# Performance work log

Hardware: AMD Instinct MI355X
Metric: run time of the kernel (lower is better)

The kernel has to match this reference:

```python
import jax, jax.numpy as jnp
import numpy as np

IN_F = 4096
OUT_F = 4096
RANK = 32
GROUP = 64  # int4 weight quantization group size along in_features


def setup_inputs() -> dict:
    key = jax.random.key(0)
    k_x, k_w, k_s, k_ld, k_lu, k_b = jax.random.split(key, 6)
    x = jax.random.normal(k_x, (4096, IN_F), dtype=jnp.float32)
    # int4 weight codes in [-8, 7], stored as int32
    qweight = jax.random.randint(k_w, (OUT_F, IN_F), -8, 8, dtype=jnp.int32)
    # per-(out_channel, group) scales
    wscale = jax.random.uniform(k_s, (OUT_F, IN_F // GROUP), dtype=jnp.float32, minval=0.01, maxval=0.05)
    # low-rank SVD correction branch (LoRA-style)
    lora_down = jax.random.normal(k_ld, (RANK, IN_F), dtype=jnp.float32) * 0.02
    lora_up = jax.random.normal(k_lu, (OUT_F, RANK), dtype=jnp.float32) * 0.02
    bias = jax.random.normal(k_b, (OUT_F,), dtype=jnp.float32) * 0.01
    return {"x": x, "qweight": qweight, "wscale": wscale,
            "lora_down": lora_down, "lora_up": lora_up, "bias": bias}


def reference(x, qweight, wscale, lora_down, lora_up, bias):
    out_f, in_f = qweight.shape
    # dequantize int4 weights group-wise: W[o, g*G+i] = q * scale[o, g]
    W = (qweight.astype(jnp.float32).reshape(out_f, in_f // GROUP, GROUP)
         * wscale[:, :, None]).reshape(out_f, in_f)
    # per-token symmetric int4 activation quantization (W4A4 main path)
    ascale = jnp.maximum(jnp.max(jnp.abs(x), axis=-1, keepdims=True), 1e-6) / 7.0
    xq = jnp.clip(jnp.round(x / ascale), -8.0, 7.0) * ascale  # fake-quantized x
    # main quantized GEMM
    main = jnp.einsum('ti,oi->to', xq, W)
    # low-rank correction uses full-precision activations
    lora = jnp.einsum('tr,or->to', jnp.einsum('ti,ri->tr', x, lora_down), lora_up)
    return main + lora + bias[None, :]
```

## Files before the change

kernel.cpp:

```cpp
#include <hip/hip_runtime.h>

typedef __bf16 bf16x8 __attribute__((ext_vector_type(8)));
typedef float f32x4 __attribute__((ext_vector_type(4)));
typedef unsigned short u16;

#define IN_F 4096
#define OUT_F 4096
#define NTOK 4096
#define RANK 32
#define KEXT 4160
#define NT 65
#define ROWB ((size_t)KEXT * 2)
#define D1 65536

__device__ __forceinline__ u16 f2bf(float f) {
  union { float f; unsigned u; } c; c.f = f;
  unsigned u = c.u;
  return (u16)((u + 0x7FFFu + ((u >> 16) & 1u)) >> 16);
}

__device__ __forceinline__ void gload_lds16(const void* g, void* l) {
  __builtin_amdgcn_global_load_lds((const __attribute__((address_space(1))) void*)g,
                                   (__attribute__((address_space(3))) void*)l,
                                   16, 0, 0);
}

__global__ __launch_bounds__(256) void prep_kernel(const float* __restrict__ x,
                                                   u16* __restrict__ A,
                                                   float* __restrict__ ascale) {
  int t = blockIdx.x;
  int tid = threadIdx.x;
  const float4* xr = (const float4*)(x + (size_t)t * IN_F);
  float4 v[4];
  float m = 0.f;
#pragma unroll
  for (int i = 0; i < 4; ++i) {
    v[i] = xr[tid + i * 256];
    m = fmaxf(m, fmaxf(fmaxf(fabsf(v[i].x), fabsf(v[i].y)),
                       fmaxf(fabsf(v[i].z), fabsf(v[i].w))));
  }
#pragma unroll
  for (int off = 32; off > 0; off >>= 1) m = fmaxf(m, __shfl_xor(m, off));
  __shared__ float wmax[4];
  if ((tid & 63) == 0) wmax[tid >> 6] = m;
  __syncthreads();
  m = fmaxf(fmaxf(wmax[0], wmax[1]), fmaxf(wmax[2], wmax[3]));
  float as = fmaxf(m, 1e-6f) / 7.f;
  float inv = 1.f / as;
  if (tid == 0) ascale[t] = as;
  u16* Ar = A + (size_t)t * KEXT;
#pragma unroll
  for (int i = 0; i < 4; ++i) {
    float q0 = fminf(fmaxf(rintf(v[i].x * inv), -8.f), 7.f);
    float q1 = fminf(fmaxf(rintf(v[i].y * inv), -8.f), 7.f);
    float q2 = fminf(fmaxf(rintf(v[i].z * inv), -8.f), 7.f);
    float q3 = fminf(fmaxf(rintf(v[i].w * inv), -8.f), 7.f);
    ushort4 u;
    u.x = f2bf(q0); u.y = f2bf(q1); u.z = f2bf(q2); u.w = f2bf(q3);
    *(ushort4*)(Ar + (size_t)(tid + i * 256) * 4) = u;
  }
  if (tid < 8) {
    ushort4 z; z.x = z.y = z.z = z.w = 0;
    *(ushort4*)(Ar + IN_F + 32 + tid * 4) = z;
  }
}

__global__ __launch_bounds__(256) void dequant_kernel(const int* __restrict__ qw,
                                                      const float* __restrict__ wscale,
                                                      const float* __restrict__ lu,
                                                      u16* __restrict__ B) {
  int o = blockIdx.x;
  int tid = threadIdx.x;
  const int4* qr = (const int4*)(qw + (size_t)o * IN_F);
  const float* sr = wscale + (size_t)o * (IN_F / 64);
  u16* Br = B + (size_t)o * KEXT;
#pragma unroll
  for (int s = 0; s < 4; ++s) {
    int e = tid + s * 256;
    int4 q = qr[e];
    float sc = sr[e >> 4];
    ushort4 u;
    u.x = f2bf((float)q.x * sc);
    u.y = f2bf((float)q.y * sc);
    u.z = f2bf((float)q.z * sc);
    u.w = f2bf((float)q.w * sc);
    *(ushort4*)(Br + (size_t)4 * e) = u;
  }
  if (tid < RANK) Br[IN_F + tid] = f2bf(lu[(size_t)o * RANK + tid]);
  if (tid < 8) {
    ushort4 z; z.x = z.y = z.z = z.w = 0;
    *(ushort4*)(Br + IN_F + 32 + tid * 4) = z;
  }
}

__global__ __launch_bounds__(256) void lorad_kernel(const float* __restrict__ x,
                                                    const float* __restrict__ ld,
                                                    float* __restrict__ tr8) {
  __shared__ float Xs[128][68];
  __shared__ float Ls[32][68];
  int b = blockIdx.x;
  int t0 = (b >> 3) * 128;
  int kbase = (b & 7) * 512;
  int tid = threadIdx.x;
  int rb = tid & 7;
  int tb = tid >> 3;
  float acc[4][4];
#pragma unroll
  for (int i = 0; i < 4; ++i)
#pragma unroll
    for (int j = 0; j < 4; ++j) acc[i][j] = 0.f;

  for (int kc = 0; kc < 512; kc += 64) {
    int k0 = kbase + kc;
    __syncthreads();
#pragma unroll
    for (int s = 0; s < 8; ++s) {
      int e = tid + s * 256;
      int row = e >> 4, c4 = (e & 15) * 4;
      float4 vv = *(const float4*)(x + (size_t)(t0 + row) * IN_F + k0 + c4);
      *(float4*)&Xs[row][c4] = vv;
    }
#pragma unroll
    for (int s = 0; s < 2; ++s) {
      int e = tid + s * 256;
      int row = e >> 4, c4 = (e & 15) * 4;
      float4 vv = *(const float4*)(ld + (size_t)row * IN_F + k0 + c4);
      *(float4*)&Ls[row][c4] = vv;
    }
    __syncthreads();
    for (int k4 = 0; k4 < 64; k4 += 4) {
      float4 lv[4], xv[4];
#pragma unroll
      for (int r = 0; r < 4; ++r) lv[r] = *(float4*)&Ls[rb + r * 8][k4];
#pragma unroll
      for (int mm = 0; mm < 4; ++mm) xv[mm] = *(float4*)&Xs[tb + mm * 32][k4];
#pragma unroll
      for (int mm = 0; mm < 4; ++mm)
#pragma unroll
        for (int r = 0; r < 4; ++r)
          acc[mm][r] += xv[mm].x * lv[r].x + xv[mm].y * lv[r].y +
                        xv[mm].z * lv[r].z + xv[mm].w * lv[r].w;
    }
  }
  float* dst = tr8 + (size_t)(b & 7) * NTOK * RANK;
#pragma unroll
  for (int mm = 0; mm < 4; ++mm)
#pragma unroll
    for (int r = 0; r < 4; ++r)
      dst[(size_t)(t0 + tb + mm * 32) * RANK + rb + r * 8] = acc[mm][r];
}

__global__ __launch_bounds__(256) void trwrite_kernel(const float* __restrict__ tr8,
                                                      const float* __restrict__ ascale,
                                                      u16* __restrict__ A) {
  int idx = blockIdx.x * 256 + threadIdx.x;
  int t = idx >> 5, r = idx & 31;
  float s = 0.f;
#pragma unroll
  for (int k = 0; k < 8; ++k) s += tr8[(size_t)k * NTOK * RANK + idx];
  A[(size_t)t * KEXT + IN_F + r] = f2bf(s / ascale[t]);
}


#define PH_SYNC() do { __builtin_amdgcn_sched_barrier(0); \
                       asm volatile("s_barrier" ::: "memory"); \
                       asm volatile("s_waitcnt lgkmcnt(0)" ::: "memory"); \
                       __builtin_amdgcn_sched_barrier(0); } while (0)
#define PH_END() do { __builtin_amdgcn_sched_barrier(0); \
                      asm volatile("s_barrier" ::: "memory"); } while (0)

#define STAGE_A(dbase, H, src) do { \
  const char* s_ = (src) + (size_t)(H) * (128 * ROWB); \
  char* l_ = smem + (dbase) + (H) * 16384 + tid * 16; \
  gload_lds16(s_, l_); \
  gload_lds16(s_ + (size_t)64 * ROWB, l_ + 8192); } while (0)

#define STAGE_B(dbase, H, src) do { \
  const char* s_ = (src) + (size_t)(H) * (128 * ROWB); \
  char* l_ = smem + (dbase) + 32768 + (H) * 16384 + tid * 16; \
  gload_lds16(s_, l_); \
  gload_lds16(s_ + (size_t)64 * ROWB, l_ + 8192); } while (0)

#define READ_A(dst, dbase, h) \
  _Pragma("unroll") for (int i = 0; i < 4; ++i) { \
    dst[i][0] = *(const bf16x8*)(smem + (dbase) + aoff + (h) * 8192 + i * 2048 + colx0); \
    dst[i][1] = *(const bf16x8*)(smem + (dbase) + aoff + (h) * 8192 + i * 2048 + colx1); }

#define READ_B(dst, dbase, uu) \
  _Pragma("unroll") for (int j = 0; j < 2; ++j) { \
    dst[j][0] = *(const bf16x8*)(smem + (dbase) + boff + (uu) * 4096 + j * 2048 + colx0); \
    dst[j][1] = *(const bf16x8*)(smem + (dbase) + boff + (uu) * 4096 + j * 2048 + colx1); }

#define MFMAQ(aS, bU, ib, jb) \
  __builtin_amdgcn_s_setprio(1); \
  _Pragma("unroll") for (int i = 0; i < 4; ++i) \
  _Pragma("unroll") for (int j = 0; j < 2; ++j) { \
    acc[(ib)+i][(jb)+j] = __builtin_amdgcn_mfma_f32_16x16x32_bf16(aS[i][0], bU[j][0], acc[(ib)+i][(jb)+j], 0, 0, 0); \
    acc[(ib)+i][(jb)+j] = __builtin_amdgcn_mfma_f32_16x16x32_bf16(aS[i][1], bU[j][1], acc[(ib)+i][(jb)+j], 0, 0, 0); } \
  __builtin_amdgcn_s_setprio(0);

__global__ __launch_bounds__(512, 2) void gemm_kernel(const u16* __restrict__ A,
                                                      const u16* __restrict__ B,
                                                      const float* __restrict__ ascale,
                                                      const float* __restrict__ bias,
                                                      float* __restrict__ out) {
  __shared__ __align__(16) char smem[131072];
  int b = blockIdx.x;
  int swz = (b & 7) * 32 + (b >> 3);
  int by = swz >> 4, bx = swz & 15;
  int tm = by * 256, tn = bx * 256;
  int tid = threadIdx.x;
  int lane = tid & 63, wid = tid >> 6;
  int wr = wid >> 2, wc = wid & 3;
  int l15 = lane & 15, l4 = lane >> 4;
  int xorb = (l15 & 7) << 4;
  int colx0 = (l4 * 16) ^ xorb;
  int colx1 = (l4 * 16 + 64) ^ xorb;
  int aoff = wr * 16384 + l15 * 128;
  int boff = 32768 + wc * 8192 + l15 * 128;

  int cb = (((tid & 7) ^ ((tid >> 3) & 7)) << 4);
  const char* ag = (const char*)A + (size_t)(tm + (tid >> 3)) * ROWB + cb;
  const char* bg = (const char*)B + (size_t)(tn + (tid >> 3)) * ROWB + cb;

  f32x4 acc[8][4];
#pragma unroll
  for (int i = 0; i < 8; ++i)
#pragma unroll
    for (int j = 0; j < 4; ++j) acc[i][j] = (f32x4){0.f, 0.f, 0.f, 0.f};

  STAGE_A(0, 0, ag);  STAGE_A(0, 1, ag);
  STAGE_B(0, 0, bg);  STAGE_B(0, 1, bg);
  STAGE_B(D1, 0, bg + 128);  STAGE_B(D1, 1, bg + 128);
  STAGE_A(D1, 0, ag + 128);
  asm volatile("s_waitcnt vmcnt(6)" ::: "memory");
  PH_END();

  const char* agT = ag;
  const char* bgT = bg;
  bf16x8 aS0[4][2], aS1[4][2], bU0[2][2], bU1[2][2];

  for (int u = 0; u < 32; ++u) {
    bool s78 = (2 * u + 3) < NT;

    READ_A(aS0, 0, 0);
    READ_B(bU0, 0, 0);
    STAGE_A(D1, 1, agT + 128);
    asm volatile("s_waitcnt lgkmcnt(8)" ::: "memory");
    PH_SYNC();
    MFMAQ(aS0, bU0, 0, 0);
    PH_END();

    READ_B(bU1, 0, 1);
    PH_SYNC();
    MFMAQ(aS0, bU1, 0, 2);
    PH_END();

    READ_A(aS1, 0, 1);
    STAGE_B(0, 0, bgT + 256);
    STAGE_B(0, 1, bgT + 256);
    PH_SYNC();
    MFMAQ(aS1, bU1, 4, 2);
    PH_END();

    STAGE_A(0, 0, agT + 256);
    STAGE_A(0, 1, agT + 256);
    asm volatile("s_waitcnt vmcnt(6)" ::: "memory");
    PH_SYNC();
    MFMAQ(aS1, bU0, 4, 0);
    PH_END();

    READ_A(aS0, D1, 0);
    READ_B(bU0, D1, 0);
    asm volatile("s_waitcnt lgkmcnt(8)" ::: "memory");
    PH_SYNC();
    MFMAQ(aS0, bU0, 0, 0);
    PH_END();

    READ_B(bU1, D1, 1);
    PH_SYNC();
    MFMAQ(aS0, bU1, 0, 2);
    PH_END();

    READ_A(aS1, D1, 1);
    if (s78) STAGE_B(D1, 0, bgT + 384);
    PH_SYNC();
    MFMAQ(aS1, bU1, 4, 2);
    PH_END();

    if (s78) {
      STAGE_B(D1, 1, bgT + 384);
      STAGE_A(D1, 0, agT + 384);
      asm volatile("s_waitcnt vmcnt(4)" ::: "memory");
    } else {
      asm volatile("s_waitcnt vmcnt(0)" ::: "memory");
    }
    PH_SYNC();
    MFMAQ(aS1, bU0, 4, 0);
    PH_END();

    agT += 256;
    bgT += 256;
  }

  READ_A(aS0, 0, 0);
  READ_B(bU0, 0, 0);
  READ_A(aS1, 0, 1);
  READ_B(bU1, 0, 1);
  MFMAQ(aS0, bU0, 0, 0);
  MFMAQ(aS0, bU1, 0, 2);
  MFMAQ(aS1, bU1, 4, 2);
  MFMAQ(aS1, bU0, 4, 0);

#pragma unroll
  for (int i = 0; i < 8; ++i) {
    int rowb = tm + wr * 128 + i * 16 + l4 * 4;
#pragma unroll
    for (int j = 0; j < 4; ++j) {
      int col = tn + wc * 64 + j * 16 + l15;
      float bv = bias[col];
#pragma unroll
      for (int q = 0; q < 4; ++q)
        out[(size_t)(rowb + q) * OUT_F + col] = acc[i][j][q] * ascale[rowb + q] + bv;
    }
  }
}

extern "C" void kernel_launch(void* const* d_in, const int* in_sizes, int n_in,
                              void* d_out, int out_size, void* d_ws, size_t ws_size,
                              hipStream_t stream) {
  const float* x = (const float*)d_in[0];
  const int* qw = (const int*)d_in[1];
  const float* wscale = (const float*)d_in[2];
  const float* ld = (const float*)d_in[3];
  const float* lu = (const float*)d_in[4];
  const float* bias = (const float*)d_in[5];
  float* out = (float*)d_out;

  char* ws = (char*)d_ws;
  const size_t szA = (size_t)NTOK * KEXT * sizeof(u16);
  const size_t szB = (size_t)OUT_F * KEXT * sizeof(u16);
  u16* Aext = (u16*)ws;
  u16* Bext = (u16*)(ws + szA);
  float* ascale = (float*)(ws + szA + szB);
  float* tr8 = (float*)(ws + szA + szB + 16384);

  prep_kernel<<<NTOK, 256, 0, stream>>>(x, Aext, ascale);
  dequant_kernel<<<OUT_F, 256, 0, stream>>>(qw, wscale, lu, Bext);
  lorad_kernel<<<256, 256, 0, stream>>>(x, ld, tr8);
  trwrite_kernel<<<NTOK * RANK / 256, 256, 0, stream>>>(tr8, ascale, Aext);
  gemm_kernel<<<(NTOK / 256) * (OUT_F / 256), 512, 0, stream>>>(Aext, Bext, ascale, bias, out);
}
```

Measured before the change: 185.5 us.

## Switch main GEMM to 32x32x16 bf16 MFMA with software-pipelined LDS reads

Replaces the 16x16x32 MFMA tiling with 32x32x16 bf16 MFMAs, so each wave issues fewer, larger matrix instructions and reuses each LDS fragment across more output. The LDS read pattern, swizzle offsets and the accumulator layout are redone to match, and the epilogue is rewritten for the 32x32 output layout. LDS fragment reads are now issued ahead of the MFMA phase that consumes the previous fragments, which is meant to hide LDS latency behind matrix math. The cost is more live registers for prefetched fragments and a reworked barrier/waitcnt schedule that could add stalls or hazards.

```diff
diff --git a/kernel.cpp b/kernel.cpp
--- a/kernel.cpp
+++ b/kernel.cpp
@@ -2,6 +2,7 @@
 
 typedef __bf16 bf16x8 __attribute__((ext_vector_type(8)));
 typedef float f32x4 __attribute__((ext_vector_type(4)));
+typedef float f32x16 __attribute__((ext_vector_type(16)));
 typedef unsigned short u16;
 
 #define IN_F 4096
@@ -181,23 +182,21 @@
   gload_lds16(s_, l_); \
   gload_lds16(s_ + (size_t)64 * ROWB, l_ + 8192); } while (0)
 
-#define READ_A(dst, dbase, h) \
-  _Pragma("unroll") for (int i = 0; i < 4; ++i) { \
-    dst[i][0] = *(const bf16x8*)(smem + (dbase) + aoff + (h) * 8192 + i * 2048 + colx0); \
-    dst[i][1] = *(const bf16x8*)(smem + (dbase) + aoff + (h) * 8192 + i * 2048 + colx1); }
-
-#define READ_B(dst, dbase, uu) \
-  _Pragma("unroll") for (int j = 0; j < 2; ++j) { \
-    dst[j][0] = *(const bf16x8*)(smem + (dbase) + boff + (uu) * 4096 + j * 2048 + colx0); \
-    dst[j][1] = *(const bf16x8*)(smem + (dbase) + boff + (uu) * 4096 + j * 2048 + colx1); }
-
-#define MFMAQ(aS, bU, ib, jb) \
+#define READ_A32(dst, dbase, h) \
+  _Pragma("unroll") for (int m2_ = 0; m2_ < 2; ++m2_) \
+  _Pragma("unroll") for (int s_ = 0; s_ < 4; ++s_) \
+    dst[m2_ * 4 + s_] = *(const bf16x8*)(smem + (dbase) + aoff + (h) * 8192 + m2_ * 4096 + colz[s_]);
+
+#define READ_B32(dst, dbase, u) \
+  _Pragma("unroll") for (int s_ = 0; s_ < 4; ++s_) \
+    dst[s_] = *(const bf16x8*)(smem + (dbase) + boff + (u) * 4096 + colz[s_]);
+
+#define MFMAQ32(aH, bH, mb, n) do { \
   __builtin_amdgcn_s_setprio(1); \
-  _Pragma("unroll") for (int i = 0; i < 4; ++i) \
-  _Pragma("unroll") for (int j = 0; j < 2; ++j) { \
-    acc[(ib)+i][(jb)+j] = __builtin_amdgcn_mfma_f32_16x16x32_bf16(aS[i][0], bU[j][0], acc[(ib)+i][(jb)+j], 0, 0, 0); \
-    acc[(ib)+i][(jb)+j] = __builtin_amdgcn_mfma_f32_16x16x32_bf16(aS[i][1], bU[j][1], acc[(ib)+i][(jb)+j], 0, 0, 0); } \
-  __builtin_amdgcn_s_setprio(0);
+  _Pragma("unroll") for (int s_ = 0; s_ < 4; ++s_) \
+  _Pragma("unroll") for (int m2_ = 0; m2_ < 2; ++m2_) \
+    acc[(mb) + m2_][n] = __builtin_amdgcn_mfma_f32_32x32x16_bf16(aH[m2_ * 4 + s_], bH[s_], acc[(mb) + m2_][n], 0, 0, 0); \
+  __builtin_amdgcn_s_setprio(0); } while (0)
 
 __global__ __launch_bounds__(512, 2) void gemm_kernel(const u16* __restrict__ A,
                                                       const u16* __restrict__ B,
@@ -212,22 +211,25 @@
   int tid = threadIdx.x;
   int lane = tid & 63, wid = tid >> 6;
   int wr = wid >> 2, wc = wid & 3;
-  int l15 = lane & 15, l4 = lane >> 4;
-  int xorb = (l15 & 7) << 4;
-  int colx0 = (l4 * 16) ^ xorb;
-  int colx1 = (l4 * 16 + 64) ^ xorb;
-  int aoff = wr * 16384 + l15 * 128;
-  int boff = 32768 + wc * 8192 + l15 * 128;
+  int l31 = lane & 31, l5 = lane >> 5;
+  int xorb = (lane & 7) << 4;
+  int colz[4];
+#pragma unroll
+  for (int s = 0; s < 4; ++s) colz[s] = (s * 32 + l5 * 16) ^ xorb;
+  int aoff = wr * 16384 + l31 * 128;
+  int boff = 32768 + wc * 8192 + l31 * 128;
 
   int cb = (((tid & 7) ^ ((tid >> 3) & 7)) << 4);
   const char* ag = (const char*)A + (size_t)(tm + (tid >> 3)) * ROWB + cb;
   const char* bg = (const char*)B + (size_t)(tn + (tid >> 3)) * ROWB + cb;
 
-  f32x4 acc[8][4];
-#pragma unroll
-  for (int i = 0; i < 8; ++i)
-#pragma unroll
-    for (int j = 0; j < 4; ++j) acc[i][j] = (f32x4){0.f, 0.f, 0.f, 0.f};
+  f32x16 acc[4][2];
+#pragma unroll
+  for (int i = 0; i < 4; ++i)
+#pragma unroll
+    for (int j = 0; j < 2; ++j)
+#pragma unroll
+      for (int e = 0; e < 16; ++e) acc[i][j][e] = 0.f;
 
   STAGE_A(0, 0, ag);  STAGE_A(0, 1, ag);
   STAGE_B(0, 0, bg);  STAGE_B(0, 1, bg);
@@ -238,54 +240,55 @@
 
   const char* agT = ag;
   const char* bgT = bg;
-  bf16x8 aS0[4][2], aS1[4][2], bU0[2][2], bU1[2][2];
+  bf16x8 aS0[8], aS1[8], bU0[4], bU1[4];
+
+  READ_A32(aS0, 0, 0);
 
   for (int u = 0; u < 32; ++u) {
     bool s78 = (2 * u + 3) < NT;
 
-    READ_A(aS0, 0, 0);
-    READ_B(bU0, 0, 0);
+    READ_B32(bU0, 0, 0);
     STAGE_A(D1, 1, agT + 128);
-    asm volatile("s_waitcnt lgkmcnt(8)" ::: "memory");
-    PH_SYNC();
-    MFMAQ(aS0, bU0, 0, 0);
-    PH_END();
-
-    READ_B(bU1, 0, 1);
-    PH_SYNC();
-    MFMAQ(aS0, bU1, 0, 2);
-    PH_END();
-
-    READ_A(aS1, 0, 1);
+    PH_SYNC();
+    READ_B32(bU1, 0, 1);
+    __builtin_amdgcn_sched_barrier(0);
+    MFMAQ32(aS0, bU0, 0, 0);
+
+    PH_SYNC();
+    READ_A32(aS1, 0, 1);
+    __builtin_amdgcn_sched_barrier(0);
+    MFMAQ32(aS0, bU1, 0, 1);
+    PH_END();
+
     STAGE_B(0, 0, bgT + 256);
     STAGE_B(0, 1, bgT + 256);
     PH_SYNC();
-    MFMAQ(aS1, bU1, 4, 2);
+    MFMAQ32(aS1, bU1, 2, 1);
     PH_END();
 
     STAGE_A(0, 0, agT + 256);
     STAGE_A(0, 1, agT + 256);
     asm volatile("s_waitcnt vmcnt(6)" ::: "memory");
     PH_SYNC();
-    MFMAQ(aS1, bU0, 4, 0);
-    PH_END();
-
-    READ_A(aS0, D1, 0);
-    READ_B(bU0, D1, 0);
-    asm volatile("s_waitcnt lgkmcnt(8)" ::: "memory");
-    PH_SYNC();
-    MFMAQ(aS0, bU0, 0, 0);
-    PH_END();
-
-    READ_B(bU1, D1, 1);
-    PH_SYNC();
-    MFMAQ(aS0, bU1, 0, 2);
-    PH_END();
-
-    READ_A(aS1, D1, 1);
+    READ_A32(aS0, D1, 0);
+    __builtin_amdgcn_sched_barrier(0);
+    MFMAQ32(aS1, bU0, 2, 0);
+
+    READ_B32(bU0, D1, 0);
+    PH_SYNC();
+    READ_B32(bU1, D1, 1);
+    __builtin_amdgcn_sched_barrier(0);
+    MFMAQ32(aS0, bU0, 0, 0);
+
+    PH_SYNC();
+    READ_A32(aS1, D1, 1);
+    __builtin_amdgcn_sched_barrier(0);
+    MFMAQ32(aS0, bU1, 0, 1);
+    PH_END();
+
     if (s78) STAGE_B(D1, 0, bgT + 384);
     PH_SYNC();
-    MFMAQ(aS1, bU1, 4, 2);
+    MFMAQ32(aS1, bU1, 2, 1);
     PH_END();
 
     if (s78) {
@@ -296,32 +299,39 @@
       asm volatile("s_waitcnt vmcnt(0)" ::: "memory");
     }
     PH_SYNC();
-    MFMAQ(aS1, bU0, 4, 0);
+    READ_A32(aS0, 0, 0);
+    __builtin_amdgcn_sched_barrier(0);
+    MFMAQ32(aS1, bU0, 2, 0);
     PH_END();
 
     agT += 256;
     bgT += 256;
   }
 
-  READ_A(aS0, 0, 0);
-  READ_B(bU0, 0, 0);
-  READ_A(aS1, 0, 1);
-  READ_B(bU1, 0, 1);
-  MFMAQ(aS0, bU0, 0, 0);
-  MFMAQ(aS0, bU1, 0, 2);
-  MFMAQ(aS1, bU1, 4, 2);
-  MFMAQ(aS1, bU0, 4, 0);
-
-#pragma unroll
-  for (int i = 0; i < 8; ++i) {
-    int rowb = tm + wr * 128 + i * 16 + l4 * 4;
-#pragma unroll
-    for (int j = 0; j < 4; ++j) {
-      int col = tn + wc * 64 + j * 16 + l15;
+  READ_B32(bU0, 0, 0);
+  READ_B32(bU1, 0, 1);
+  READ_A32(aS1, 0, 1);
+  asm volatile("s_waitcnt lgkmcnt(0)" ::: "memory");
+  __builtin_amdgcn_sched_barrier(0);
+  MFMAQ32(aS0, bU0, 0, 0);
+  MFMAQ32(aS0, bU1, 0, 1);
+  MFMAQ32(aS1, bU1, 2, 1);
+  MFMAQ32(aS1, bU0, 2, 0);
+
+#pragma unroll
+  for (int m = 0; m < 4; ++m) {
+#pragma unroll
+    for (int n = 0; n < 2; ++n) {
+      int col = tn + wc * 64 + n * 32 + l31;
       float bv = bias[col];
 #pragma unroll
-      for (int q = 0; q < 4; ++q)
-        out[(size_t)(rowb + q) * OUT_F + col] = acc[i][j][q] * ascale[rowb + q] + bv;
+      for (int g = 0; g < 4; ++g) {
+#pragma unroll
+        for (int q = 0; q < 4; ++q) {
+          int row = tm + wr * 128 + m * 32 + 8 * g + 4 * l5 + q;
+          out[(size_t)row * OUT_F + col] = acc[m][n][4 * g + q] * ascale[row] + bv;
+        }
+      }
     }
   }
 }
```

Result: slower. 190.8 us (+2.9%).
